# Optimization experiments

Hardware: AMD Instinct MI355X
Metric: run time of the kernel (lower is better)

The kernel has to match this reference:

```python
import jax, jax.numpy as jnp
import numpy as np

F, V, NF, T = 240, 100000, 16, 2048


def _mesh_normalize(v):
    # v: (B, N, 3)
    mmax = jnp.max(v, axis=1, keepdims=True)
    mmin = jnp.min(v, axis=1, keepdims=True)
    v = v - (mmax + mmin) / 2
    big = jnp.max(v.reshape(v.shape[0], -1), axis=1)
    return v / big[:, None, None]


def _qmult(q1, q0):
    # Hamilton product, matches the torch qmult coefficient layout (wxyz)
    w0, x0, y0, z0 = q0[..., 0], q0[..., 1], q0[..., 2], q0[..., 3]
    w1, x1, y1, z1 = q1[..., 0], q1[..., 1], q1[..., 2], q1[..., 3]
    return jnp.stack([
        -x1 * x0 - y1 * y0 - z1 * z0 + w1 * w0,
         x1 * w0 + y1 * z0 - z1 * y0 + w1 * x0,
        -x1 * z0 + y1 * w0 + z1 * x0 + w1 * y0,
         x1 * y0 - y1 * x0 + z1 * w0 + w1 * z0], axis=-1)


def setup_inputs() -> dict:
    key = jax.random.key(0)
    k1, k2, k3, k4, k5 = jax.random.split(key, 5)
    # parameters initialized as in __init__ plus small perturbation (as after some training)
    tr = jnp.zeros((1, 1, F, 3)).at[0, 0, 0, 2].set(2.0) + 0.01 * jax.random.normal(k1, (1, 1, F, 3))
    q = jnp.zeros((1, F, 4)).at[:, :, 0].set(1.0) + 0.01 * jax.random.normal(k2, (1, F, 4))
    vp = 0.01 * jax.random.normal(k3, (1, V, 3))
    tex = jnp.ones((1, NF, T, T)) + 0.1 * jax.random.normal(k4, (1, NF, T, T))
    iv = _mesh_normalize(jax.random.normal(k5, (1, V, 3)))
    off = jnp.zeros((1, 1, F, 7)).at[:, :, :, 3].set(1.0)  # identity quaternion offsets, zero translation offsets
    of = jnp.arange(F, dtype=jnp.int32)
    return dict(translation_p=tr, quaternion_p=q, vertices_p=vp, texture_map=tex,
                ivertices=iv, offsets=off, opt_frames=of)


def reference(translation_p, quaternion_p, vertices_p, texture_map, ivertices, offsets, opt_frames):
    # opt_frames == arange(F): every frame is optimized, so no detach branch fires
    # and the per-frame python loop vectorizes (no cross-frame data dependence in outputs).
    qf = quaternion_p[0]                                      # (F, 4)
    qn = qf / jnp.linalg.norm(qf, axis=-1, keepdims=True)
    offq = offsets[0, 0, :, 3:]                               # (F, 4)
    offn = offq / jnp.linalg.norm(offq, axis=-1, keepdims=True)
    qprod = _qmult(qn, offn)                                  # (F, 4)
    # frame 0 uses the bare normalized quaternion; frames >=1 include the offset product
    q_all = jnp.concatenate([qn[:1], qprod[1:]], axis=0)      # (F, 4)
    t_all = jnp.concatenate(
        [translation_p[:, :, :1], translation_p[:, :, 1:] + offsets[:, :, 1:, :3]], axis=2)  # (1,1,F,3)

    of = opt_frames
    w = (of - jnp.concatenate([of[:1], of[:-1]])).astype(t_all.dtype)  # (K,)

    # tdiff = wghts * comp_tran_diff(translation[0,0,opt_frames])
    t = t_all[0, 0][of]                                       # (K, 3)
    vd = jnp.abs(t[1:] - t[:-1])
    vd = jnp.where(vd < 0.2, jnp.zeros_like(vd), vd)
    vd = jnp.concatenate([jnp.zeros_like(vd[:1]), vd], axis=0)
    tdiff = w * jnp.linalg.norm(vd, axis=1)

    # qdiff: first entry is qdist(quaternion0, quaternion0) with quaternion0 = last-loop value
    qlast = q_all[-1]
    d0 = 1.0 - jnp.sum(qlast * qlast) ** 2
    qa = q_all[of[1:] - 1]
    qb = q_all[of[1:]]
    kd = 1.0 - jnp.sum(qa * qb, axis=-1) ** 2
    qdiff = w * jnp.concatenate([d0[None], kd], axis=0)

    # predict_vertices=True, mesh_normalize=True
    vertices = _mesh_normalize(ivertices + vertices_p)

    # features == 'deep' -> raw texture map (no sigmoid)
    return (t_all[:, :, of], q_all[None][:, of], vertices, texture_map, tdiff, qdiff)
```

## Files before the change

### kernel.cpp

```cpp
#include <hip/hip_runtime.h>
#include <float.h>
#include <math.h>

#define F_MAX 512
#define RED_BLOCKS 128

typedef float f4 __attribute__((ext_vector_type(4)));

__global__ __launch_bounds__(256) void minmax_frames_kernel(
    const float* __restrict__ iv, const float* __restrict__ vp, int V,
    float* __restrict__ partial,
    const float* __restrict__ tr,
    const float* __restrict__ q,
    const float* __restrict__ off,
    const int*   __restrict__ of,
    float* __restrict__ out_t,
    float* __restrict__ out_q,
    float* __restrict__ out_td,
    float* __restrict__ out_qd,
    int F)
{
    const int t = threadIdx.x;

    float mx0=-FLT_MAX, mx1=-FLT_MAX, mx2=-FLT_MAX;
    float mn0= FLT_MAX, mn1= FLT_MAX, mn2= FLT_MAX;
    for (int v = blockIdx.x * blockDim.x + t; v < V;
         v += gridDim.x * blockDim.x) {
        float a0 = iv[3*v+0] + vp[3*v+0];
        float a1 = iv[3*v+1] + vp[3*v+1];
        float a2 = iv[3*v+2] + vp[3*v+2];
        mx0 = fmaxf(mx0, a0); mn0 = fminf(mn0, a0);
        mx1 = fmaxf(mx1, a1); mn1 = fminf(mn1, a1);
        mx2 = fmaxf(mx2, a2); mn2 = fminf(mn2, a2);
    }
    __shared__ float s[256][6];
    s[t][0]=mx0; s[t][1]=mx1; s[t][2]=mx2; s[t][3]=mn0; s[t][4]=mn1; s[t][5]=mn2;
    __syncthreads();
    for (int w = 128; w >= 1; w >>= 1) {
        if (t < w) {
            s[t][0] = fmaxf(s[t][0], s[t+w][0]);
            s[t][1] = fmaxf(s[t][1], s[t+w][1]);
            s[t][2] = fmaxf(s[t][2], s[t+w][2]);
            s[t][3] = fminf(s[t][3], s[t+w][3]);
            s[t][4] = fminf(s[t][4], s[t+w][4]);
            s[t][5] = fminf(s[t][5], s[t+w][5]);
        }
        __syncthreads();
    }
    if (t == 0) {
        #pragma unroll
        for (int k = 0; k < 6; ++k) partial[blockIdx.x*6 + k] = s[0][k];
    }

    if (blockIdx.x != 0) return;

    __shared__ float qall[F_MAX][4];
    __shared__ float tall[F_MAX][3];

    for (int f = t; f < F; f += blockDim.x) {
        float w1 = q[4*f+0], x1 = q[4*f+1], y1 = q[4*f+2], z1 = q[4*f+3];
        float n1 = sqrtf(w1*w1 + x1*x1 + y1*y1 + z1*z1);
        w1 /= n1; x1 /= n1; y1 /= n1; z1 /= n1;
        float w0 = off[7*f+3], x0 = off[7*f+4], y0 = off[7*f+5], z0 = off[7*f+6];
        float n0 = sqrtf(w0*w0 + x0*x0 + y0*y0 + z0*z0);
        w0 /= n0; x0 /= n0; y0 /= n0; z0 /= n0;
        float pw = -x1*x0 - y1*y0 - z1*z0 + w1*w0;
        float px =  x1*w0 + y1*z0 - z1*y0 + w1*x0;
        float py = -x1*z0 + y1*w0 + z1*x0 + w1*y0;
        float pz =  x1*y0 - y1*x0 + z1*w0 + w1*z0;
        if (f == 0) { pw = w1; px = x1; py = y1; pz = z1; }
        qall[f][0] = pw; qall[f][1] = px; qall[f][2] = py; qall[f][3] = pz;
        float o0 = 0.f, o1 = 0.f, o2 = 0.f;
        if (f >= 1) { o0 = off[7*f+0]; o1 = off[7*f+1]; o2 = off[7*f+2]; }
        tall[f][0] = tr[3*f+0] + o0;
        tall[f][1] = tr[3*f+1] + o1;
        tall[f][2] = tr[3*f+2] + o2;
    }
    __syncthreads();

    for (int j = t; j < F; j += blockDim.x) {
        const int fj = of[j];
        out_t[3*j+0] = tall[fj][0];
        out_t[3*j+1] = tall[fj][1];
        out_t[3*j+2] = tall[fj][2];
        out_q[4*j+0] = qall[fj][0];
        out_q[4*j+1] = qall[fj][1];
        out_q[4*j+2] = qall[fj][2];
        out_q[4*j+3] = qall[fj][3];

        float wj = (j == 0) ? 0.0f : (float)(of[j] - of[j-1]);

        float td = 0.0f;
        if (j >= 1) {
            const int fp = of[j-1];
            float ssum = 0.0f;
            #pragma unroll
            for (int c = 0; c < 3; ++c) {
                float d = fabsf(tall[fj][c] - tall[fp][c]);
                if (d < 0.2f) d = 0.0f;
                ssum += d * d;
            }
            td = wj * sqrtf(ssum);
        }
        out_td[j] = td;

        float qd;
        if (j == 0) {
            float sm = qall[F-1][0]*qall[F-1][0] + qall[F-1][1]*qall[F-1][1]
                     + qall[F-1][2]*qall[F-1][2] + qall[F-1][3]*qall[F-1][3];
            qd = wj * (1.0f - sm*sm);
        } else {
            int ia = fj - 1;
            if (ia < 0) ia += F;
            float sm = qall[ia][0]*qall[fj][0] + qall[ia][1]*qall[fj][1]
                     + qall[ia][2]*qall[fj][2] + qall[ia][3]*qall[fj][3];
            qd = wj * (1.0f - sm*sm);
        }
        out_qd[j] = qd;
    }
}

__global__ __launch_bounds__(256) void finalize_kernel(
    const float* __restrict__ partial, int nb, float* __restrict__ params)
{
    float mx0=-FLT_MAX, mx1=-FLT_MAX, mx2=-FLT_MAX;
    float mn0= FLT_MAX, mn1= FLT_MAX, mn2= FLT_MAX;
    const int t = threadIdx.x;
    for (int b = t; b < nb; b += blockDim.x) {
        mx0 = fmaxf(mx0, partial[6*b+0]);
        mx1 = fmaxf(mx1, partial[6*b+1]);
        mx2 = fmaxf(mx2, partial[6*b+2]);
        mn0 = fminf(mn0, partial[6*b+3]);
        mn1 = fminf(mn1, partial[6*b+4]);
        mn2 = fminf(mn2, partial[6*b+5]);
    }
    __shared__ float s[256][6];
    s[t][0]=mx0; s[t][1]=mx1; s[t][2]=mx2; s[t][3]=mn0; s[t][4]=mn1; s[t][5]=mn2;
    __syncthreads();
    for (int w = 128; w >= 1; w >>= 1) {
        if (t < w) {
            s[t][0] = fmaxf(s[t][0], s[t+w][0]);
            s[t][1] = fmaxf(s[t][1], s[t+w][1]);
            s[t][2] = fmaxf(s[t][2], s[t+w][2]);
            s[t][3] = fminf(s[t][3], s[t+w][3]);
            s[t][4] = fminf(s[t][4], s[t+w][4]);
            s[t][5] = fminf(s[t][5], s[t+w][5]);
        }
        __syncthreads();
    }
    if (t == 0) {
        float cx = (s[0][0] + s[0][3]) * 0.5f;
        float cy = (s[0][1] + s[0][4]) * 0.5f;
        float cz = (s[0][2] + s[0][5]) * 0.5f;
        float big = fmaxf(fmaxf(s[0][0] - cx, s[0][1] - cy), s[0][2] - cz);
        params[0] = cx; params[1] = cy; params[2] = cz; params[3] = big;
    }
}

__global__ __launch_bounds__(256) void copy_norm_kernel(
    const f4* __restrict__ tex, f4* __restrict__ out_tex, long n_tex4,
    const float* __restrict__ iv, const float* __restrict__ vp,
    const float* __restrict__ params, f4* __restrict__ out_v, int nv4)
{
    const long stride = (long)gridDim.x * blockDim.x;
    const long tid0   = (long)blockIdx.x * blockDim.x + threadIdx.x;

    for (long i = tid0; i < nv4; i += stride) {
        const float c0 = params[0], c1 = params[1], c2 = params[2];
        const float big = params[3];
        f4 a = ((const f4*)iv)[i] + ((const f4*)vp)[i];
        f4 r;
        const int base = (int)(i * 4);
        #pragma unroll
        for (int j = 0; j < 4; ++j) {
            const int comp = (base + j) % 3;
            const float c = (comp == 0) ? c0 : ((comp == 1) ? c1 : c2);
            r[j] = (a[j] - c) / big;
        }
        out_v[i] = r;
    }

    for (long i = tid0; i < n_tex4; i += stride) {
        f4 v = __builtin_nontemporal_load(&tex[i]);
        __builtin_nontemporal_store(v, &out_tex[i]);
    }
}

extern "C" void kernel_launch(void* const* d_in, const int* in_sizes, int n_in,
                              void* d_out, int out_size, void* d_ws, size_t ws_size,
                              hipStream_t stream) {
    const float* tr  = (const float*)d_in[0];
    const float* q   = (const float*)d_in[1];
    const float* vp  = (const float*)d_in[2];
    const float* tex = (const float*)d_in[3];
    const float* iv  = (const float*)d_in[4];
    const float* off = (const float*)d_in[5];
    const int*   of  = (const int*)d_in[6];

    const int F    = in_sizes[6];
    const int nt   = in_sizes[0];
    const int nq   = in_sizes[1];
    const int nv   = in_sizes[2];
    const int ntex = in_sizes[3];
    const int V    = nv / 3;

    float* out     = (float*)d_out;
    float* out_t   = out;
    float* out_q   = out + nt;
    float* out_v   = out + nt + nq;
    float* out_tex = out + nt + nq + nv;
    float* out_td  = out + (size_t)nt + nq + nv + ntex;
    float* out_qd  = out_td + F;

    float* partial = (float*)d_ws;
    float* params  = partial + RED_BLOCKS * 6;

    minmax_frames_kernel<<<RED_BLOCKS, 256, 0, stream>>>(
        iv, vp, V, partial, tr, q, off, of, out_t, out_q, out_td, out_qd, F);
    finalize_kernel<<<1, 256, 0, stream>>>(partial, RED_BLOCKS, params);

    const long n_tex4 = (long)ntex / 4;
    const int  nv4    = nv / 4;
    copy_norm_kernel<<<2048, 256, 0, stream>>>(
        (const f4*)tex, (f4*)out_tex, n_tex4, iv, vp, params, (f4*)out_v, nv4);
}
```

Before: 109.4 us.

## Fuse finalize into copy kernel, vectorize min/max reduction, block-contiguous texture copy

```diff
diff --git a/kernel.cpp b/kernel.cpp
--- a/kernel.cpp
+++ b/kernel.cpp
@@ -3,12 +3,13 @@
 #include <math.h>
 
 #define F_MAX 512
-#define RED_BLOCKS 128
+#define RED_BLOCKS 64
+#define COPY_GRID 4096
 
 typedef float f4 __attribute__((ext_vector_type(4)));
 
 __global__ __launch_bounds__(256) void minmax_frames_kernel(
-    const float* __restrict__ iv, const float* __restrict__ vp, int V,
+    const f4* __restrict__ iv4, const f4* __restrict__ vp4, int nv4,
     float* __restrict__ partial,
     const float* __restrict__ tr,
     const float* __restrict__ q,
@@ -24,14 +25,29 @@
 
     float mx0=-FLT_MAX, mx1=-FLT_MAX, mx2=-FLT_MAX;
     float mn0= FLT_MAX, mn1= FLT_MAX, mn2= FLT_MAX;
-    for (int v = blockIdx.x * blockDim.x + t; v < V;
-         v += gridDim.x * blockDim.x) {
-        float a0 = iv[3*v+0] + vp[3*v+0];
-        float a1 = iv[3*v+1] + vp[3*v+1];
-        float a2 = iv[3*v+2] + vp[3*v+2];
-        mx0 = fmaxf(mx0, a0); mn0 = fminf(mn0, a0);
-        mx1 = fmaxf(mx1, a1); mn1 = fminf(mn1, a1);
-        mx2 = fmaxf(mx2, a2); mn2 = fminf(mn2, a2);
+    const int gstride = gridDim.x * blockDim.x;
+    for (int i = blockIdx.x * blockDim.x + t; i < nv4; i += gstride) {
+        f4 a = iv4[i] + vp4[i];
+        switch (i % 3) {
+        case 0:
+            mx0=fmaxf(mx0,a[0]); mn0=fminf(mn0,a[0]);
+            mx1=fmaxf(mx1,a[1]); mn1=fminf(mn1,a[1]);
+            mx2=fmaxf(mx2,a[2]); mn2=fminf(mn2,a[2]);
+            mx0=fmaxf(mx0,a[3]); mn0=fminf(mn0,a[3]);
+            break;
+        case 1:
+            mx1=fmaxf(mx1,a[0]); mn1=fminf(mn1,a[0]);
+            mx2=fmaxf(mx2,a[1]); mn2=fminf(mn2,a[1]);
+            mx0=fmaxf(mx0,a[2]); mn0=fminf(mn0,a[2]);
+            mx1=fmaxf(mx1,a[3]); mn1=fminf(mn1,a[3]);
+            break;
+        default:
+            mx2=fmaxf(mx2,a[0]); mn2=fminf(mn2,a[0]);
+            mx0=fmaxf(mx0,a[1]); mn0=fminf(mn0,a[1]);
+            mx1=fmaxf(mx1,a[2]); mn1=fminf(mn1,a[2]);
+            mx2=fmaxf(mx2,a[3]); mn2=fminf(mn2,a[3]);
+            break;
+        }
     }
     __shared__ float s[256][6];
     s[t][0]=mx0; s[t][1]=mx1; s[t][2]=mx2; s[t][3]=mn0; s[t][4]=mn1; s[t][5]=mn2;
@@ -120,70 +136,56 @@
     }
 }
 
-__global__ __launch_bounds__(256) void finalize_kernel(
-    const float* __restrict__ partial, int nb, float* __restrict__ params)
+__global__ __launch_bounds__(256) void copy_finalize_norm_kernel(
+    const f4* __restrict__ tex, f4* __restrict__ out_tex, long n_tex4,
+    const float* __restrict__ partial,
+    const f4* __restrict__ iv4, const f4* __restrict__ vp4,
+    f4* __restrict__ out_v, int nv4)
 {
-    float mx0=-FLT_MAX, mx1=-FLT_MAX, mx2=-FLT_MAX;
-    float mn0= FLT_MAX, mn1= FLT_MAX, mn2= FLT_MAX;
     const int t = threadIdx.x;
-    for (int b = t; b < nb; b += blockDim.x) {
-        mx0 = fmaxf(mx0, partial[6*b+0]);
-        mx1 = fmaxf(mx1, partial[6*b+1]);
-        mx2 = fmaxf(mx2, partial[6*b+2]);
-        mn0 = fminf(mn0, partial[6*b+3]);
-        mn1 = fminf(mn1, partial[6*b+4]);
-        mn2 = fminf(mn2, partial[6*b+5]);
-    }
-    __shared__ float s[256][6];
-    s[t][0]=mx0; s[t][1]=mx1; s[t][2]=mx2; s[t][3]=mn0; s[t][4]=mn1; s[t][5]=mn2;
-    __syncthreads();
-    for (int w = 128; w >= 1; w >>= 1) {
-        if (t < w) {
-            s[t][0] = fmaxf(s[t][0], s[t+w][0]);
-            s[t][1] = fmaxf(s[t][1], s[t+w][1]);
-            s[t][2] = fmaxf(s[t][2], s[t+w][2]);
-            s[t][3] = fminf(s[t][3], s[t+w][3]);
-            s[t][4] = fminf(s[t][4], s[t+w][4]);
-            s[t][5] = fminf(s[t][5], s[t+w][5]);
-        }
-        __syncthreads();
-    }
-    if (t == 0) {
-        float cx = (s[0][0] + s[0][3]) * 0.5f;
-        float cy = (s[0][1] + s[0][4]) * 0.5f;
-        float cz = (s[0][2] + s[0][5]) * 0.5f;
-        float big = fmaxf(fmaxf(s[0][0] - cx, s[0][1] - cy), s[0][2] - cz);
-        params[0] = cx; params[1] = cy; params[2] = cz; params[3] = big;
-    }
-}
-
-__global__ __launch_bounds__(256) void copy_norm_kernel(
-    const f4* __restrict__ tex, f4* __restrict__ out_tex, long n_tex4,
-    const float* __restrict__ iv, const float* __restrict__ vp,
-    const float* __restrict__ params, f4* __restrict__ out_v, int nv4)
-{
-    const long stride = (long)gridDim.x * blockDim.x;
-    const long tid0   = (long)blockIdx.x * blockDim.x + threadIdx.x;
-
-    for (long i = tid0; i < nv4; i += stride) {
-        const float c0 = params[0], c1 = params[1], c2 = params[2];
-        const float big = params[3];
-        f4 a = ((const f4*)iv)[i] + ((const f4*)vp)[i];
+
+    const int gvid = blockIdx.x * blockDim.x + t;
+    if (gvid < nv4) {
+        float mx0=-FLT_MAX, mx1=-FLT_MAX, mx2=-FLT_MAX;
+        float mn0= FLT_MAX, mn1= FLT_MAX, mn2= FLT_MAX;
+        for (int b = 0; b < RED_BLOCKS; ++b) {
+            mx0 = fmaxf(mx0, partial[6*b+0]);
+            mx1 = fmaxf(mx1, partial[6*b+1]);
+            mx2 = fmaxf(mx2, partial[6*b+2]);
+            mn0 = fminf(mn0, partial[6*b+3]);
+            mn1 = fminf(mn1, partial[6*b+4]);
+            mn2 = fminf(mn2, partial[6*b+5]);
+        }
+        const float c0 = (mx0 + mn0) * 0.5f;
+        const float c1 = (mx1 + mn1) * 0.5f;
+        const float c2 = (mx2 + mn2) * 0.5f;
+        const float big = fmaxf(fmaxf(mx0 - c0, mx1 - c1), mx2 - c2);
+
+        f4 a = iv4[gvid] + vp4[gvid];
         f4 r;
-        const int base = (int)(i * 4);
-        #pragma unroll
-        for (int j = 0; j < 4; ++j) {
-            const int comp = (base + j) % 3;
-            const float c = (comp == 0) ? c0 : ((comp == 1) ? c1 : c2);
-            r[j] = (a[j] - c) / big;
-        }
-        out_v[i] = r;
-    }
-
-    for (long i = tid0; i < n_tex4; i += stride) {
-        f4 v = __builtin_nontemporal_load(&tex[i]);
-        __builtin_nontemporal_store(v, &out_tex[i]);
-    }
+        switch (gvid % 3) {
+        case 0:
+            r[0]=(a[0]-c0)/big; r[1]=(a[1]-c1)/big;
+            r[2]=(a[2]-c2)/big; r[3]=(a[3]-c0)/big; break;
+        case 1:
+            r[0]=(a[0]-c1)/big; r[1]=(a[1]-c2)/big;
+            r[2]=(a[2]-c0)/big; r[3]=(a[3]-c1)/big; break;
+        default:
+            r[0]=(a[0]-c2)/big; r[1]=(a[1]-c0)/big;
+            r[2]=(a[2]-c1)/big; r[3]=(a[3]-c2)/big; break;
+        }
+        out_v[gvid] = r;
+    }
+
+    const long gsz   = (long)gridDim.x * blockDim.x;
+    const long iters = n_tex4 / gsz;
+    const long base  = (long)blockIdx.x * (blockDim.x * iters) + t;
+    #pragma unroll 4
+    for (long k = 0; k < iters; ++k) {
+        out_tex[base + k * blockDim.x] = tex[base + k * blockDim.x];
+    }
+    const long g = gsz * iters + (long)blockIdx.x * blockDim.x + t;
+    if (g < n_tex4) out_tex[g] = tex[g];
 }
 
 extern "C" void kernel_launch(void* const* d_in, const int* in_sizes, int n_in,
@@ -202,7 +204,6 @@
     const int nq   = in_sizes[1];
     const int nv   = in_sizes[2];
     const int ntex = in_sizes[3];
-    const int V    = nv / 3;
 
     float* out     = (float*)d_out;
     float* out_t   = out;
@@ -213,14 +214,15 @@
     float* out_qd  = out_td + F;
 
     float* partial = (float*)d_ws;
-    float* params  = partial + RED_BLOCKS * 6;
+
+    const int nv4 = nv / 4;
 
     minmax_frames_kernel<<<RED_BLOCKS, 256, 0, stream>>>(
-        iv, vp, V, partial, tr, q, off, of, out_t, out_q, out_td, out_qd, F);
-    finalize_kernel<<<1, 256, 0, stream>>>(partial, RED_BLOCKS, params);
+        (const f4*)iv, (const f4*)vp, nv4, partial,
+        tr, q, off, of, out_t, out_q, out_td, out_qd, F);
 
     const long n_tex4 = (long)ntex / 4;
-    const int  nv4    = nv / 4;
-    copy_norm_kernel<<<2048, 256, 0, stream>>>(
-        (const f4*)tex, (f4*)out_tex, n_tex4, iv, vp, params, (f4*)out_v, nv4);
+    copy_finalize_norm_kernel<<<COPY_GRID, 256, 0, stream>>>(
+        (const f4*)tex, (f4*)out_tex, n_tex4,
+        partial, (const f4*)iv, (const f4*)vp, (f4*)out_v, nv4);
 }
```

New measurement: 117.7 us. 7.5% more time.
